# Optimization experiments

Measured on AMD Instinct MI355X. Metric: run time of the kernel, lower is better.

Reference implementation:

```python
import jax, jax.numpy as jnp
import numpy as np

B, T, D = 8, 4097, 512
H = 8
WIN = 64


def setup_inputs() -> dict:
    key = jax.random.key(0)
    k1, k2, k3 = jax.random.split(key, 3)
    x = jax.random.normal(k1, (B, T, D), dtype=jnp.float32)
    w_qkv = jax.random.normal(k2, (D, 3 * D), dtype=jnp.float32) * 0.02
    w_out = jax.random.normal(k3, (D, D), dtype=jnp.float32) * 0.02
    return {"x": x, "w_qkv": w_qkv, "w_out": w_out}


def reference(x, w_qkv, w_out):
    b, t, d_model = x.shape
    d = d_model // H
    scale = d ** (-0.5)
    nw = (t - 1) // WIN  # number of full windows over bbox tokens

    qkv = x @ w_qkv  # [B, T, 3D]
    q, k, v = jnp.split(qkv, 3, axis=-1)
    # [B, H, T, d]
    to_heads = lambda z: z.reshape(b, t, H, d).transpose(0, 2, 1, 3)
    q, k, v = to_heads(q), to_heads(k), to_heads(v)

    # global token (index 0) attends to ALL tokens
    q0 = q[:, :, :1]  # [B, H, 1, d]
    attn0 = jax.nn.softmax(jnp.einsum('bhqd,bhkd->bhqk', q0, k) * scale, axis=-1)
    out0 = jnp.einsum('bhqk,bhkd->bhqd', attn0, v)  # [B, H, 1, d]

    # bbox tokens: local attention within non-overlapping windows (no global token in keys)
    qw = q[:, :, 1:].reshape(b, H, nw, WIN, d)
    kw = k[:, :, 1:].reshape(b, H, nw, WIN, d)
    vw = v[:, :, 1:].reshape(b, H, nw, WIN, d)
    s = jnp.einsum('bhnqd,bhnkd->bhnqk', qw, kw) * scale
    attn = jax.nn.softmax(s, axis=-1)
    ow = jnp.einsum('bhnqk,bhnkd->bhnqd', attn, vw).reshape(b, H, t - 1, d)

    out = jnp.concatenate([out0, ow], axis=2)  # [B, H, T, d]
    out = out.transpose(0, 2, 1, 3).reshape(b, t, d_model)
    return out @ w_out
```

## Files before the change

kernel.cpp:

```cpp
#include <hip/hip_runtime.h>
#include <hip/hip_bf16.h>
#include <cstdint>
#include <cstddef>

using bf16 = __hip_bfloat16;
using short8 = __attribute__((ext_vector_type(8))) short;
using f32x4  = __attribute__((ext_vector_type(4))) float;

constexpr int Bc = 8;
constexpr int Tc = 4097;
constexpr int Dc = 512;
constexpr int Hc = 8;
constexpr int Mrows = Bc * Tc;
constexpr int Mpad2 = 33024;
constexpr int NW = 64;

__device__ __forceinline__ float bf2f(unsigned short u) {
    union { unsigned int i; float f; } v;
    v.i = ((unsigned int)u) << 16;
    return v.f;
}

__device__ __forceinline__ unsigned short f2b(float f) {
    union { float f; unsigned int i; } u; u.f = f;
    unsigned int r = u.i + 0x7FFFu + ((u.i >> 16) & 1u);
    return (unsigned short)(r >> 16);
}

__device__ __forceinline__ void gload_lds16(const void* g, void* l) {
    __builtin_amdgcn_global_load_lds(
        (const __attribute__((address_space(1))) void*)g,
        (__attribute__((address_space(3))) void*)l, 16, 0, 0);
}

__global__ __launch_bounds__(256)
void k_cvt_x(const float* __restrict__ x, bf16* __restrict__ xb)
{
    size_t i8 = ((size_t)blockIdx.x * 256 + threadIdx.x) * 8;
    if (i8 >= (size_t)Mpad2 * 512) return;
    union { short s[8]; short8 v; } o;
    if (i8 < (size_t)Mrows * 512) {
        float4 v0 = *(const float4*)(x + i8);
        float4 v1 = *(const float4*)(x + i8 + 4);
        o.s[0] = (short)f2b(v0.x); o.s[1] = (short)f2b(v0.y);
        o.s[2] = (short)f2b(v0.z); o.s[3] = (short)f2b(v0.w);
        o.s[4] = (short)f2b(v1.x); o.s[5] = (short)f2b(v1.y);
        o.s[6] = (short)f2b(v1.z); o.s[7] = (short)f2b(v1.w);
    } else {
        o.v = short8{0,0,0,0,0,0,0,0};
    }
    *(short8*)((short*)xb + i8) = o.v;
}

__global__ __launch_bounds__(256)
void k_cvt_wT(const float* __restrict__ w, bf16* __restrict__ wT, int K, int N)
{
    __shared__ float t[32][33];
    int bn = blockIdx.x * 32, bk = blockIdx.y * 32;
    int tx = threadIdx.x & 31, ty = threadIdx.x >> 5;
    #pragma unroll
    for (int j = 0; j < 4; ++j)
        t[ty + j * 8][tx] = w[(size_t)(bk + ty + j * 8) * N + bn + tx];
    __syncthreads();
    #pragma unroll
    for (int j = 0; j < 4; ++j)
        wT[(size_t)(bn + ty + j * 8) * K + bk + tx] =
            __float2bfloat16(t[tx][ty + j * 8]);
}

template <typename OutT, int NT>
__global__ __launch_bounds__(256)
void k_gemm_dbuf(const bf16* __restrict__ A, const bf16* __restrict__ Bt,
                 OutT* __restrict__ C, int Mlim)
{
    constexpr int N = NT * 128;
    __shared__ short lds[32768];

    const int tid = threadIdx.x;
    const int lane = tid & 63, wave = tid >> 6;
    const int lo = lane & 15, g = lane >> 4;
    const int wr = wave >> 1, wc = wave & 1;

    const int nwg = 257 * NT;
    const int orig = blockIdx.x;
    const int qq = nwg >> 3, rr = nwg & 7;
    const int xc = orig & 7, o8 = orig >> 3;
    const int swz = (xc < rr ? xc * (qq + 1) : rr * (qq + 1) + (xc - rr) * qq) + o8;
    const int bm = (swz / NT) * 128, bn = (swz % NT) * 128;

    const bf16* aSrc[4]; const bf16* bSrc[4];
    int dstOff[4];
    #pragma unroll
    for (int i = 0; i < 4; ++i) {
        int d = i * 256 + tid;
        int row = d >> 3, c = d & 7;
        int ck = (c - row) & 7;
        aSrc[i] = A  + (size_t)(bm + row) * 512 + ck * 8;
        bSrc[i] = Bt + (size_t)(bn + row) * 512 + ck * 8;
        dstOff[i] = d * 8;
    }

    auto STAGE = [&](int kt) {
        const int bb = (kt & 1) * 16384;
        #pragma unroll
        for (int i = 0; i < 4; ++i)
            gload_lds16(aSrc[i] + kt * 64, lds + bb + dstOff[i]);
        #pragma unroll
        for (int i = 0; i < 4; ++i)
            gload_lds16(bSrc[i] + kt * 64, lds + bb + 8192 + dstOff[i]);
    };

    const int colk[2] = { (g + (lo & 7)) & 7, (g + 4 + (lo & 7)) & 7 };
    const int arow0 = wr * 64 + lo;
    const int brow0 = wc * 64 + lo;

    f32x4 acc[4][4] = {};

    STAGE(0);
    STAGE(1);
    asm volatile("s_waitcnt vmcnt(8)" ::: "memory");
    __builtin_amdgcn_s_barrier();

    for (int t = 0; t < 8; ++t) {
        const short* bufA = lds + (t & 1) * 16384;
        const short* bufB = bufA + 8192;

        #pragma unroll
        for (int ks = 0; ks < 2; ++ks) {
            const int col = colk[ks];
            short8 af[4], bfr[4];
            #pragma unroll
            for (int mi = 0; mi < 4; ++mi)
                af[mi] = *(const short8*)(bufA + (arow0 + mi * 16) * 64 + col * 8);
            #pragma unroll
            for (int ni = 0; ni < 4; ++ni)
                bfr[ni] = *(const short8*)(bufB + (brow0 + ni * 16) * 64 + col * 8);
            __builtin_amdgcn_s_setprio(1);
            #pragma unroll
            for (int mi = 0; mi < 4; ++mi)
                #pragma unroll
                for (int ni = 0; ni < 4; ++ni)
                    acc[mi][ni] = __builtin_amdgcn_mfma_f32_16x16x32_bf16(
                        bfr[ni], af[mi], acc[mi][ni], 0, 0, 0);
            __builtin_amdgcn_s_setprio(0);
        }

        asm volatile("s_waitcnt lgkmcnt(0)" ::: "memory");
        __builtin_amdgcn_s_barrier();
        if (t < 6) {
            STAGE(t + 2);
            asm volatile("s_waitcnt vmcnt(8)" ::: "memory");
            __builtin_amdgcn_s_barrier();
        } else if (t == 6) {
            asm volatile("s_waitcnt vmcnt(0)" ::: "memory");
            __builtin_amdgcn_s_barrier();
        }
    }

    #pragma unroll
    for (int mi = 0; mi < 4; ++mi) {
        int m = bm + wr * 64 + mi * 16 + lo;
        if (m < Mlim) {
            #pragma unroll
            for (int ni = 0; ni < 4; ++ni) {
                int n = bn + wc * 64 + ni * 16 + g * 4;
                if constexpr (sizeof(OutT) == 2) {
                    ushort4 o = { f2b(acc[mi][ni][0]), f2b(acc[mi][ni][1]),
                                  f2b(acc[mi][ni][2]), f2b(acc[mi][ni][3]) };
                    *(ushort4*)((bf16*)C + (size_t)m * N + n) = o;
                } else {
                    float4 o = { acc[mi][ni][0], acc[mi][ni][1],
                                 acc[mi][ni][2], acc[mi][ni][3] };
                    *(float4*)((float*)C + (size_t)m * N + n) = o;
                }
            }
        }
    }
}

__global__ __launch_bounds__(256)
void k_attn_win(const bf16* __restrict__ qkv, bf16* __restrict__ aout,
                float* __restrict__ part)
{
    __shared__ __attribute__((aligned(16))) unsigned short pS[64 * 64];
    __shared__ __attribute__((aligned(16))) unsigned short vT[64 * 64];
    __shared__ float q0s[64];
    __shared__ float pTok[64];
    __shared__ float oPart[4][64];

    const int n = blockIdx.x, h = blockIdx.y, b = blockIdx.z;
    const int tid = threadIdx.x;
    const int wave = tid >> 6, lane = tid & 63;
    const int lo = lane & 15, g = lane >> 4;

    const bf16* base = qkv + ((size_t)b * Tc + 1 + (size_t)n * 64) * 1536 + h * 64;
    const bf16* kbase = base + 512;
    const bf16* vbase = base + 1024;

    {
        const int key = tid & 63;
        const int d0 = (tid >> 6) * 16;
        const bf16* vp = vbase + (size_t)key * 1536 + d0;
        ushort4 u[4];
        #pragma unroll
        for (int q = 0; q < 4; ++q) u[q] = *(const ushort4*)(vp + q * 4);
        const unsigned short vals[16] = {
            u[0].x, u[0].y, u[0].z, u[0].w, u[1].x, u[1].y, u[1].z, u[1].w,
            u[2].x, u[2].y, u[2].z, u[2].w, u[3].x, u[3].y, u[3].z, u[3].w };
        #pragma unroll
        for (int j = 0; j < 16; ++j) {
            int d = d0 + j;
            int byteoff = d * 128 + ((key * 2) ^ ((d & 7) << 4));
            *(unsigned short*)((char*)vT + byteoff) = vals[j];
        }
    }

    if (tid < 64)
        q0s[tid] = bf2f(*(const unsigned short*)
            (qkv + (size_t)b * Tc * 1536 + h * 64 + tid));

    short8 qf[2];
    {
        const bf16* qp = base + (size_t)(wave * 16 + lo) * 1536 + g * 8;
        qf[0] = *(const short8*)(qp);
        qf[1] = *(const short8*)(qp + 32);
    }

    f32x4 sacc[4] = {};
    #pragma unroll
    for (int ni = 0; ni < 4; ++ni) {
        const bf16* kp = kbase + (size_t)(ni * 16 + lo) * 1536 + g * 8;
        short8 k0 = *(const short8*)(kp);
        short8 k1 = *(const short8*)(kp + 32);
        sacc[ni] = __builtin_amdgcn_mfma_f32_16x16x32_bf16(qf[0], k0, sacc[ni], 0, 0, 0);
        sacc[ni] = __builtin_amdgcn_mfma_f32_16x16x32_bf16(qf[1], k1, sacc[ni], 0, 0, 0);
    }

    __syncthreads();

    float m_w = 0.f, s_w = 0.f;
    if (wave == 0) {
        const bf16* kp = kbase + (size_t)lane * 1536;
        float l = 0.f;
        #pragma unroll
        for (int d8 = 0; d8 < 8; ++d8) {
            short8 kv = *(const short8*)(kp + d8 * 8);
            #pragma unroll
            for (int e = 0; e < 8; ++e)
                l = fmaf(q0s[d8 * 8 + e], bf2f((unsigned short)kv[e]), l);
        }
        l *= 0.125f;
        float mm = l;
        #pragma unroll
        for (int off = 1; off < 64; off <<= 1) mm = fmaxf(mm, __shfl_xor(mm, off));
        float p = __expf(l - mm);
        float ss = p;
        #pragma unroll
        for (int off = 1; off < 64; off <<= 1) ss += __shfl_xor(ss, off);
        pTok[lane] = p;
        m_w = mm; s_w = ss;
    }

    float pv[4][4];
    float inv[4];
    #pragma unroll
    for (int r = 0; r < 4; ++r) {
        float m = fmaxf(fmaxf(sacc[0][r], sacc[1][r]),
                        fmaxf(sacc[2][r], sacc[3][r])) * 0.125f;
        m = fmaxf(m, __shfl_xor(m, 1));
        m = fmaxf(m, __shfl_xor(m, 2));
        m = fmaxf(m, __shfl_xor(m, 4));
        m = fmaxf(m, __shfl_xor(m, 8));
        float s = 0.f;
        #pragma unroll
        for (int ni = 0; ni < 4; ++ni) {
            float e = __expf(sacc[ni][r] * 0.125f - m);
            pv[ni][r] = e;
            s += e;
        }
        s += __shfl_xor(s, 1);
        s += __shfl_xor(s, 2);
        s += __shfl_xor(s, 4);
        s += __shfl_xor(s, 8);
        inv[r] = 1.f / s;
    }

    #pragma unroll
    for (int ni = 0; ni < 4; ++ni) {
        #pragma unroll
        for (int r = 0; r < 4; ++r) {
            int qrow = wave * 16 + g * 4 + r;
            int col = ni * 16 + lo;
            int byteoff = qrow * 128 + ((col * 2) ^ ((qrow & 7) << 4));
            *(unsigned short*)((char*)pS + byteoff) = f2b(pv[ni][r]);
        }
    }
    __syncthreads();

    f32x4 oacc[4] = {};
    #pragma unroll
    for (int s = 0; s < 2; ++s) {
        int arow2 = wave * 16 + lo;
        int abyte = arow2 * 128 + (((s * 32 + g * 8) * 2) ^ ((arow2 & 7) << 4));
        short8 pa = *(const short8*)((const char*)pS + abyte);
        #pragma unroll
        for (int nd = 0; nd < 4; ++nd) {
            int d = nd * 16 + lo;
            int bbyte = d * 128 + (((s * 32 + g * 8) * 2) ^ ((d & 7) << 4));
            short8 vb = *(const short8*)((const char*)vT + bbyte);
            oacc[nd] = __builtin_amdgcn_mfma_f32_16x16x32_bf16(pa, vb, oacc[nd], 0, 0, 0);
        }
    }

    {
        const int d = tid & 63, qq = tid >> 6;
        float po = 0.f;
        #pragma unroll
        for (int j16 = 0; j16 < 16; ++j16) {
            int j = qq * 16 + j16;
            int byteoff = d * 128 + ((j * 2) ^ ((d & 7) << 4));
            po = fmaf(pTok[j],
                      bf2f(*(const unsigned short*)((const char*)vT + byteoff)),
                      po);
        }
        oPart[qq][d] = po;
    }

    #pragma unroll
    for (int nd = 0; nd < 4; ++nd) {
        #pragma unroll
        for (int r = 0; r < 4; ++r) {
            int t = 1 + n * 64 + wave * 16 + g * 4 + r;
            aout[((size_t)b * Tc + t) * Dc + h * 64 + nd * 16 + lo] =
                __float2bfloat16(oacc[nd][r] * inv[r]);
        }
    }

    __syncthreads();

    if (tid < 64) {
        float o0 = oPart[0][tid] + oPart[1][tid] + oPart[2][tid] + oPart[3][tid];
        float* pout = part + ((size_t)(b * Hc + h) * NW + n) * 66;
        pout[tid] = o0;
        if (tid == 0) { pout[64] = m_w; pout[65] = s_w; }
    }
}

__global__ __launch_bounds__(64)
void k_tok0_reduce(const float* __restrict__ part, const bf16* __restrict__ qkv,
                   bf16* __restrict__ aout)
{
    const int h = blockIdx.x, b = blockIdx.y;
    const int lane = threadIdx.x;
    const float* basep = part + (size_t)(b * Hc + h) * NW * 66;
    const bf16* qrow = qkv + (size_t)b * Tc * 1536 + h * 64;

    float l0 = bf2f(*(const unsigned short*)(qrow + lane)) *
               bf2f(*(const unsigned short*)(qrow + 512 + lane));
    #pragma unroll
    for (int off = 1; off < 64; off <<= 1) l0 += __shfl_xor(l0, off);
    l0 *= 0.125f;

    float M = basep[lane * 66 + 64];
    #pragma unroll
    for (int off = 1; off < 64; off <<= 1) M = fmaxf(M, __shfl_xor(M, off));
    M = fmaxf(M, l0);

    float S = 0.f, o = 0.f;
    for (int c = 0; c < NW; ++c) {
        const float* pp = basep + c * 66;
        float w = __expf(pp[64] - M);
        S += pp[65] * w;
        o = fmaf(pp[lane], w, o);
    }
    float p0 = __expf(l0 - M);
    S += p0;
    o = fmaf(p0, bf2f(*(const unsigned short*)(qrow + 1024 + lane)), o);

    aout[(size_t)b * Tc * Dc + h * 64 + lane] = __float2bfloat16(o / S);
}

extern "C" void kernel_launch(void* const* d_in, const int* in_sizes, int n_in,
                              void* d_out, int out_size, void* d_ws, size_t ws_size,
                              hipStream_t stream)
{
    const float* x     = (const float*)d_in[0];
    const float* w_qkv = (const float*)d_in[1];
    const float* w_out = (const float*)d_in[2];
    float* out = (float*)d_out;

    bf16* qkv = (bf16*)d_ws;
    bf16* xa  = qkv + (size_t)Mrows * 1536;
    bf16* wqT = xa  + (size_t)Mpad2 * 512;
    bf16* woT = wqT + (size_t)1536 * 512;
    float* part = (float*)wqT;

    {
        int nblk = (int)(((size_t)Mpad2 * 512 / 8 + 255) / 256);
        k_cvt_x<<<nblk, 256, 0, stream>>>(x, xa);
    }
    k_cvt_wT<<<dim3(48, 16), 256, 0, stream>>>(w_qkv, wqT, 512, 1536);
    k_cvt_wT<<<dim3(16, 16), 256, 0, stream>>>(w_out, woT, 512, 512);

    k_gemm_dbuf<bf16, 12><<<257 * 12, 256, 0, stream>>>(xa, wqT, qkv, Mrows);

    k_attn_win<<<dim3(64, Hc, Bc), 256, 0, stream>>>(qkv, xa, part);
    k_tok0_reduce<<<dim3(Hc, Bc), dim3(64), 0, stream>>>(part, qkv, xa);

    k_gemm_dbuf<float, 4><<<257 * 4, 256, 0, stream>>>(xa, woT, out, Mrows);
}
```

Baseline: 167.0 us.

## Use 256x256-tile 8-wave GEMM with ping-pong pipeline for QKV projection

```diff
diff --git a/kernel.cpp b/kernel.cpp
--- a/kernel.cpp
+++ b/kernel.cpp
@@ -68,6 +68,130 @@
             __float2bfloat16(t[tx][ty + j * 8]);
 }
 
+template <int NT>
+__global__ __launch_bounds__(512, 1)
+void k_gemm_8p(const bf16* __restrict__ A, const bf16* __restrict__ Bt,
+               bf16* __restrict__ C, int Mlim)
+{
+    constexpr int N = NT * 256;
+    __shared__ short lds[65536];
+
+    const int tid = threadIdx.x;
+    const int lane = tid & 63, wave = tid >> 6;
+    const int lo = lane & 15, g = lane >> 4;
+    const int wr = wave >> 2, wc = wave & 3;
+
+    const int nwg = 129 * NT;
+    const int orig = blockIdx.x;
+    const int qq = nwg >> 3, rr = nwg & 7;
+    const int xc = orig & 7, o8 = orig >> 3;
+    const int swz = (xc < rr ? xc * (qq + 1) : rr * (qq + 1) + (xc - rr) * qq) + o8;
+    const int bm = (swz / NT) * 256, bn = (swz % NT) * 256;
+
+    const bf16* srcU[8];
+    int dstU[8];
+    {
+        const int lr = tid >> 3, c = tid & 7;
+        #pragma unroll
+        for (int u = 0; u < 8; ++u) {
+            int row;
+            const bf16* gbase;
+            int dbase;
+            if (u < 4) {
+                row = u * 64 + lr;
+                gbase = Bt + (size_t)(bn + row) * 512;
+                dbase = 16384 + row * 64;
+            } else {
+                int qa = u - 4;
+                row = (lr < 32) ? (qa * 32 + lr) : (128 + qa * 32 + (lr - 32));
+                gbase = A + (size_t)(bm + row) * 512;
+                dbase = row * 64;
+            }
+            int ck = (c - row) & 7;
+            srcU[u] = gbase + ck * 8;
+            dstU[u] = dbase + c * 8;
+        }
+    }
+
+    const int colk[2] = { (g + (lo & 7)) & 7, (g + 4 + (lo & 7)) & 7 };
+    const int browBase = wc * 64 + lo;
+
+    f32x4 acc[8][4] = {};
+
+    #pragma unroll
+    for (int u = 0; u < 8; ++u)
+        gload_lds16(srcU[u], lds + dstU[u]);
+    asm volatile("s_waitcnt vmcnt(2)" ::: "memory");
+    asm volatile("s_barrier" ::: "memory");
+
+    for (int t = 0; t < 8; ++t) {
+        const short* buf = lds + (t & 1) * 32768;
+        const int sb = ((t + 1) & 1) * 32768;
+        short8 bfr[4][2];
+
+        #pragma unroll
+        for (int p = 0; p < 4; ++p) {
+            short8 af[2][2];
+            #pragma unroll
+            for (int m2 = 0; m2 < 2; ++m2)
+                #pragma unroll
+                for (int ks = 0; ks < 2; ++ks)
+                    af[m2][ks] = *(const short8*)(
+                        buf + (wr * 128 + (2 * p + m2) * 16 + lo) * 64 + colk[ks] * 8);
+            if (p == 0) {
+                #pragma unroll
+                for (int ni = 0; ni < 4; ++ni)
+                    #pragma unroll
+                    for (int ks = 0; ks < 2; ++ks)
+                        bfr[ni][ks] = *(const short8*)(
+                            buf + 16384 + (browBase + ni * 16) * 64 + colk[ks] * 8);
+            }
+
+            if (t < 7) {
+                gload_lds16(srcU[2 * p]     + (t + 1) * 64, lds + sb + dstU[2 * p]);
+                gload_lds16(srcU[2 * p + 1] + (t + 1) * 64, lds + sb + dstU[2 * p + 1]);
+            }
+
+            if (p == 1) {
+                if (t < 7) asm volatile("s_waitcnt vmcnt(4)" ::: "memory");
+                else       asm volatile("s_waitcnt vmcnt(0)" ::: "memory");
+            }
+            if (p == 3 && t < 7)
+                asm volatile("s_waitcnt vmcnt(2)" ::: "memory");
+
+            asm volatile("s_barrier" ::: "memory");
+            asm volatile("s_waitcnt lgkmcnt(0)" ::: "memory");
+            __builtin_amdgcn_sched_barrier(0);
+
+            __builtin_amdgcn_s_setprio(1);
+            #pragma unroll
+            for (int m2 = 0; m2 < 2; ++m2)
+                #pragma unroll
+                for (int ni = 0; ni < 4; ++ni)
+                    #pragma unroll
+                    for (int ks = 0; ks < 2; ++ks)
+                        acc[2 * p + m2][ni] = __builtin_amdgcn_mfma_f32_16x16x32_bf16(
+                            bfr[ni][ks], af[m2][ks], acc[2 * p + m2][ni], 0, 0, 0);
+            __builtin_amdgcn_s_setprio(0);
+            asm volatile("s_barrier" ::: "memory");
+        }
+    }
+
+    #pragma unroll
+    for (int mi = 0; mi < 8; ++mi) {
+        int m = bm + wr * 128 + mi * 16 + lo;
+        if (m < Mlim) {
+            #pragma unroll
+            for (int ni = 0; ni < 4; ++ni) {
+                int n = bn + wc * 64 + ni * 16 + g * 4;
+                ushort4 o = { f2b(acc[mi][ni][0]), f2b(acc[mi][ni][1]),
+                              f2b(acc[mi][ni][2]), f2b(acc[mi][ni][3]) };
+                *(ushort4*)(C + (size_t)m * N + n) = o;
+            }
+        }
+    }
+}
+
 template <typename OutT, int NT>
 __global__ __launch_bounds__(256)
 void k_gemm_dbuf(const bf16* __restrict__ A, const bf16* __restrict__ Bt,
@@ -402,7 +526,7 @@
     k_cvt_wT<<<dim3(48, 16), 256, 0, stream>>>(w_qkv, wqT, 512, 1536);
     k_cvt_wT<<<dim3(16, 16), 256, 0, stream>>>(w_out, woT, 512, 512);
 
-    k_gemm_dbuf<bf16, 12><<<257 * 12, 256, 0, stream>>>(xa, wqT, qkv, Mrows);
+    k_gemm_8p<6><<<129 * 6, 512, 0, stream>>>(xa, wqT, qkv, Mrows);
 
     k_attn_win<<<dim3(64, Hc, Bc), 256, 0, stream>>>(qkv, xa, part);
     k_tok0_reduce<<<dim3(Hc, Bc), dim3(64), 0, stream>>>(part, qkv, xa);
```

Result: slower. 185.1 us (+10.8%).

## Add QKV GEMM kernel loading B fragments directly from global into registers

Applied to the files above, without the earlier changes.

```diff
diff --git a/kernel.cpp b/kernel.cpp
--- a/kernel.cpp
+++ b/kernel.cpp
@@ -68,6 +68,123 @@
             __float2bfloat16(t[tx][ty + j * 8]);
 }
 
+template <int NT>
+__global__ __launch_bounds__(256)
+void k_gemm_bd(const bf16* __restrict__ A, const bf16* __restrict__ Bt,
+               bf16* __restrict__ C, int Mlim)
+{
+    constexpr int N = NT * 128;
+    __shared__ short lds[16384];
+
+    const int tid = threadIdx.x;
+    const int lane = tid & 63, wave = tid >> 6;
+    const int lo = lane & 15, g = lane >> 4;
+    const int wr = wave >> 1, wc = wave & 1;
+
+    const int nwg = 257 * NT;
+    const int orig = blockIdx.x;
+    const int qq = nwg >> 3, rr = nwg & 7;
+    const int xc = orig & 7, o8 = orig >> 3;
+    const int swz = (xc < rr ? xc * (qq + 1) : rr * (qq + 1) + (xc - rr) * qq) + o8;
+    const int bm = (swz / NT) * 128, bn = (swz % NT) * 128;
+
+    const bf16* aSrc[4];
+    int dstOff[4];
+    #pragma unroll
+    for (int i = 0; i < 4; ++i) {
+        int d = i * 256 + tid;
+        int row = d >> 3, c = d & 7;
+        int ck = (c - row) & 7;
+        aSrc[i] = A + (size_t)(bm + row) * 512 + ck * 8;
+        dstOff[i] = d * 8;
+    }
+
+    auto STAGE = [&](int kt) {
+        const int bb = (kt & 1) * 8192;
+        #pragma unroll
+        for (int i = 0; i < 4; ++i)
+            gload_lds16(aSrc[i] + kt * 64, lds + bb + dstOff[i]);
+    };
+
+    const bf16* bPtr[4];
+    #pragma unroll
+    for (int ni = 0; ni < 4; ++ni)
+        bPtr[ni] = Bt + (size_t)(bn + wc * 64 + ni * 16 + lo) * 512 + g * 8;
+
+    const int colk[2] = { (g + (lo & 7)) & 7, (g + 4 + (lo & 7)) & 7 };
+    const int arow0 = wr * 64 + lo;
+
+    f32x4 acc[4][4] = {};
+    short8 b0[4][2], b1[4][2];
+
+    STAGE(0);
+    STAGE(1);
+    asm volatile("" ::: "memory");
+    #pragma unroll
+    for (int ni = 0; ni < 4; ++ni) {
+        b0[ni][0] = *(const short8*)(bPtr[ni]);
+        b0[ni][1] = *(const short8*)(bPtr[ni] + 32);
+    }
+    asm volatile("s_waitcnt vmcnt(12)" ::: "memory");
+    asm volatile("s_barrier" ::: "memory");
+
+    auto STEP = [&](int t, short8 (&bc)[4][2], short8 (&bnx)[4][2]) {
+        if (t < 7) {
+            #pragma unroll
+            for (int ni = 0; ni < 4; ++ni) {
+                bnx[ni][0] = *(const short8*)(bPtr[ni] + (t + 1) * 64);
+                bnx[ni][1] = *(const short8*)(bPtr[ni] + (t + 1) * 64 + 32);
+            }
+        }
+        const short* bufA = lds + (t & 1) * 8192;
+        #pragma unroll
+        for (int ks = 0; ks < 2; ++ks) {
+            short8 af[4];
+            #pragma unroll
+            for (int mi = 0; mi < 4; ++mi)
+                af[mi] = *(const short8*)(bufA + (arow0 + mi * 16) * 64 + colk[ks] * 8);
+            __builtin_amdgcn_s_setprio(1);
+            #pragma unroll
+            for (int mi = 0; mi < 4; ++mi)
+                #pragma unroll
+                for (int ni = 0; ni < 4; ++ni)
+                    acc[mi][ni] = __builtin_amdgcn_mfma_f32_16x16x32_bf16(
+                        bc[ni][ks], af[mi], acc[mi][ni], 0, 0, 0);
+            __builtin_amdgcn_s_setprio(0);
+        }
+        asm volatile("s_waitcnt lgkmcnt(0)" ::: "memory");
+        asm volatile("s_barrier" ::: "memory");
+        if (t < 6) {
+            STAGE(t + 2);
+            asm volatile("s_waitcnt vmcnt(12)" ::: "memory");
+            asm volatile("s_barrier" ::: "memory");
+        } else if (t == 6) {
+            asm volatile("s_waitcnt vmcnt(8)" ::: "memory");
+            asm volatile("s_barrier" ::: "memory");
+        }
+    };
+
+    #pragma unroll
+    for (int tt = 0; tt < 4; ++tt) {
+        STEP(2 * tt,     b0, b1);
+        STEP(2 * tt + 1, b1, b0);
+    }
+
+    #pragma unroll
+    for (int mi = 0; mi < 4; ++mi) {
+        int m = bm + wr * 64 + mi * 16 + lo;
+        if (m < Mlim) {
+            #pragma unroll
+            for (int ni = 0; ni < 4; ++ni) {
+                int n = bn + wc * 64 + ni * 16 + g * 4;
+                ushort4 o = { f2b(acc[mi][ni][0]), f2b(acc[mi][ni][1]),
+                              f2b(acc[mi][ni][2]), f2b(acc[mi][ni][3]) };
+                *(ushort4*)(C + (size_t)m * N + n) = o;
+            }
+        }
+    }
+}
+
 template <typename OutT, int NT>
 __global__ __launch_bounds__(256)
 void k_gemm_dbuf(const bf16* __restrict__ A, const bf16* __restrict__ Bt,
@@ -402,7 +519,7 @@
     k_cvt_wT<<<dim3(48, 16), 256, 0, stream>>>(w_qkv, wqT, 512, 1536);
     k_cvt_wT<<<dim3(16, 16), 256, 0, stream>>>(w_out, woT, 512, 512);
 
-    k_gemm_dbuf<bf16, 12><<<257 * 12, 256, 0, stream>>>(xa, wqT, qkv, Mrows);
+    k_gemm_bd<12><<<257 * 12, 256, 0, stream>>>(xa, wqT, qkv, Mrows);
 
     k_attn_win<<<dim3(64, Hc, Bc), 256, 0, stream>>>(qkv, xa, part);
     k_tok0_reduce<<<dim3(Hc, Bc), dim3(64), 0, stream>>>(part, qkv, xa);
```

Result: slower. 229.8 us (+37.6%).
